# Optimization experiments

Measured on AMD Instinct MI355X. Metric: run time of the kernel, lower is better.

The kernel has to match this reference:

```python
import jax, jax.numpy as jnp
import numpy as np

PAD_TOKEN = -2.0
EPS = 1e-6
NEG_INF = -1.0e9


def _layer_norm(x, gamma, beta):
    mu = jnp.mean(x, axis=-1, keepdims=True)
    var = jnp.mean(jnp.square(x - mu), axis=-1, keepdims=True)
    return (x - mu) * jax.lax.rsqrt(var + EPS) * gamma + beta


def setup_inputs() -> dict:
    key = jax.random.key(0)
    ks = jax.random.split(key, 10)
    B, N, M, D, H, E, O = 128, 32, 384, 256, 8, 32, 256
    S = N + M
    x_pmhc = jax.random.normal(ks[0], (B, S, D), jnp.float32)
    # masks hold raw token values; PAD_TOKEN marks padding positions
    p_len = jax.random.randint(ks[1], (B,), 8, N + 1)
    m_len = jax.random.randint(ks[2], (B,), M // 2, M + 1)
    p_mask = jnp.where(jnp.arange(N)[None, :] < p_len[:, None], 1.0, PAD_TOKEN).astype(jnp.float32)
    m_mask = jnp.where(jnp.arange(M)[None, :] < m_len[:, None], 1.0, PAD_TOKEN).astype(jnp.float32)
    # learned params (keras random_normal init stddev=0.05; random_uniform in [-0.05, 0.05])
    q_proj = 0.05 * jax.random.normal(ks[3], (H, D, E), jnp.float32)
    k_proj = 0.05 * jax.random.normal(ks[4], (H, D, E), jnp.float32)
    v_proj = 0.05 * jax.random.normal(ks[5], (H, D, E), jnp.float32)
    g_proj = jax.random.uniform(ks[6], (H, D, E), jnp.float32, -0.05, 0.05)
    out_w = 0.05 * jax.random.normal(ks[7], (H * E, O), jnp.float32)
    out_b = jnp.zeros((O,), jnp.float32)
    ln1_g = jnp.ones((D,), jnp.float32)
    ln1_b = jnp.zeros((D,), jnp.float32)
    ln2_g = jnp.ones((O,), jnp.float32)
    ln2_b = jnp.zeros((O,), jnp.float32)
    return dict(x_pmhc=x_pmhc, p_mask=p_mask, m_mask=m_mask,
                q_proj=q_proj, k_proj=k_proj, v_proj=v_proj, g_proj=g_proj,
                out_w=out_w, out_b=out_b,
                ln1_g=ln1_g, ln1_b=ln1_b, ln2_g=ln2_g, ln2_b=ln2_b)


def _mask_2d(p, m):
    # p: [B,N] in {0,1}, m: [B,M] in {0,1}
    B, N = p.shape
    M = m.shape[1]
    cross_pm = p[:, :, None] * m[:, None, :]          # [B,N,M]
    cross_mp = m[:, :, None] * p[:, None, :]          # [B,M,N]
    top = jnp.concatenate([jnp.zeros((B, N, N), p.dtype), cross_pm], axis=2)
    bot = jnp.concatenate([cross_mp, jnp.zeros((B, M, M), p.dtype)], axis=2)
    return jnp.concatenate([top, bot], axis=1)        # [B,S,S]


def reference(x_pmhc, p_mask, m_mask, q_proj, k_proj, v_proj, g_proj,
              out_w, out_b, ln1_g, ln1_b, ln2_g, ln2_b):
    H, _, E = q_proj.shape
    B, S, _ = x_pmhc.shape
    scale = 1.0 / jnp.sqrt(jnp.asarray(E, jnp.float32))
    x = _layer_norm(x_pmhc, ln1_g, ln1_b)
    p = jnp.where(p_mask == PAD_TOKEN, 0.0, 1.0)
    m = jnp.where(m_mask == PAD_TOKEN, 0.0, 1.0)
    q = jnp.einsum('bxd,hde->bhxe', x, q_proj)
    k = jnp.einsum('bxd,hde->bhxe', x, k_proj)
    v = jnp.einsum('bxd,hde->bhxe', x, v_proj)
    g = jnp.einsum('bxd,hde->bhxe', x, g_proj)
    att = jnp.einsum('bhxe,bhye->bhxy', q, k) * scale          # [B,H,S,S]
    mask2d = _mask_2d(p, m)                                     # [B,S,S]
    att = jax.nn.softmax(att + ((1.0 - mask2d) * NEG_INF)[:, None], axis=-1)
    att = att * mask2d[:, None]
    out = jnp.einsum('bhxy,bhye->bhxe', att, v)
    out = out * jax.nn.sigmoid(g)
    out = out.transpose(0, 2, 1, 3).reshape(B, S, H * E)
    out = out @ out_w + out_b
    return _layer_norm(out, ln2_g, ln2_b)
```

## Files before the change

kernel.cpp:

```cpp
#include <hip/hip_runtime.h>

typedef unsigned short u16;
typedef __bf16 bf16x8 __attribute__((ext_vector_type(8)));
typedef float f32x4 __attribute__((ext_vector_type(4)));

#define B_    128
#define S_    416
#define NPEP  32
#define MMHC  384
#define D_    256
#define H_    8
#define E_    32
#define O_    256
#define BS_   (B_ * S_)

#define PAD_TOK (-2.0f)
#define SCALE_E 0.17677669529663687f

typedef const __attribute__((address_space(1))) void cg_void;
typedef __attribute__((address_space(3))) void lds_void;

__device__ __forceinline__ float bf2f(u16 u) {
  union { unsigned int i; float f; } x; x.i = ((unsigned int)u) << 16; return x.f;
}
__device__ __forceinline__ u16 f2bf(float f) {
  union { float f; unsigned int i; } x; x.f = f;
  unsigned int i = x.i;
  return (u16)((i + 0x7FFFu + ((i >> 16) & 1u)) >> 16);
}
__device__ __forceinline__ unsigned pk2bf(float lo, float hi) {
  return (unsigned)f2bf(lo) | ((unsigned)f2bf(hi) << 16);
}

__global__ __launch_bounds__(256)
void pack_w(const float* __restrict__ q, const float* __restrict__ k,
            const float* __restrict__ v, const float* __restrict__ g,
            const float* __restrict__ ow, u16* __restrict__ WT, u16* __restrict__ WoT) {
  const int bx = blockIdx.x, t = threadIdx.x;
  if (bx < 1024) {
    const int col = bx;
    const int p = col >> 8, h = (col >> 5) & 7, e = col & 31;
    const float* src = (p == 0) ? q : (p == 1) ? k : (p == 2) ? v : g;
    WT[col * 256 + t] = f2bf(src[(h * 256 + t) * 32 + e]);
  } else {
    const int n = bx - 1024;
    WoT[n * 256 + t] = f2bf(ow[t * 256 + n]);
  }
}

__global__ __launch_bounds__(256)
void ln_f2b(const float* __restrict__ inp, u16* __restrict__ out,
            const float* __restrict__ gam, const float* __restrict__ bet) {
  const int w = threadIdx.x >> 6, lane = threadIdx.x & 63;
  const size_t row = (size_t)blockIdx.x * 4 + w;
  const float4 u = *((const float4*)inp + row * 64 + lane);
  const float x0 = u.x, x1 = u.y, x2 = u.z, x3 = u.w;
  float sum = (x0 + x1) + (x2 + x3);
  float ss  = (x0 * x0 + x1 * x1) + (x2 * x2 + x3 * x3);
  #pragma unroll
  for (int off = 32; off; off >>= 1) {
    sum += __shfl_xor(sum, off);
    ss  += __shfl_xor(ss, off);
  }
  const float mean = sum * 0.00390625f;
  float var = ss * 0.00390625f - mean * mean;
  var = fmaxf(var, 0.0f);
  const float rs = rsqrtf(var + 1e-6f);
  const float4 g4 = *((const float4*)gam + lane);
  const float4 b4 = *((const float4*)bet + lane);
  ushort4 r;
  r.x = f2bf((x0 - mean) * rs * g4.x + b4.x);
  r.y = f2bf((x1 - mean) * rs * g4.y + b4.y);
  r.z = f2bf((x2 - mean) * rs * g4.z + b4.z);
  r.w = f2bf((x3 - mean) * rs * g4.w + b4.w);
  *((ushort4*)out + row * 64 + lane) = r;
}

__global__ __launch_bounds__(256, 2)
void gemm_qkvg(const u16* __restrict__ A, const u16* __restrict__ BT,
               u16* __restrict__ Qh, u16* __restrict__ Kh,
               u16* __restrict__ Vh, u16* __restrict__ Gh) {
  __shared__ __attribute__((aligned(16))) u16 As[128 * 64];
  __shared__ __attribute__((aligned(16))) u16 Bs[128 * 64];
  const int L = blockIdx.x;
  const int m0 = ((L & 7) + 8 * (L >> 6)) * 128;
  const int n0 = ((L >> 3) & 7) * 128;
  const int tid = threadIdx.x;
  const int lane = tid & 63;
  const int w = tid >> 6;
  const int wr = (w >> 1) * 64;
  const int wc = (w & 1) * 64;
  const int mi = lane & 15;
  const int quad = lane >> 4;
  const int rseg = lane >> 3;
  const int gcol = (lane & 7) ^ rseg;
  f32x4 acc[4][4] = {};
  for (int kc = 0; kc < 256; kc += 64) {
    __syncthreads();
    #pragma unroll
    for (int j = 0; j < 4; ++j) {
      const int seg = w * 4 + j;
      const int r = seg * 8 + rseg;
      const u16* ga = &A[(size_t)(m0 + r) * 256 + kc + gcol * 8];
      __builtin_amdgcn_global_load_lds((cg_void*)ga, (lds_void*)&As[seg * 512], 16, 0, 0);
      const u16* gb = &BT[(size_t)(n0 + r) * 256 + kc + gcol * 8];
      __builtin_amdgcn_global_load_lds((cg_void*)gb, (lds_void*)&Bs[seg * 512], 16, 0, 0);
    }
    __syncthreads();
    #pragma unroll
    for (int kt = 0; kt < 2; ++kt) {
      bf16x8 a[4], bb[4];
      #pragma unroll
      for (int i = 0; i < 4; ++i) {
        const int m = wr + i * 16 + mi;
        const int pg = (kt * 4 + quad) ^ (mi & 7);
        a[i] = *(const bf16x8*)&As[m * 64 + pg * 8];
      }
      #pragma unroll
      for (int i = 0; i < 4; ++i) {
        const int n = wc + i * 16 + mi;
        const int pg = (kt * 4 + quad) ^ (mi & 7);
        bb[i] = *(const bf16x8*)&Bs[n * 64 + pg * 8];
      }
      #pragma unroll
      for (int i = 0; i < 4; ++i)
        #pragma unroll
        for (int jn = 0; jn < 4; ++jn)
          acc[i][jn] = __builtin_amdgcn_mfma_f32_16x16x32_bf16(a[i], bb[jn], acc[i][jn], 0, 0, 0);
    }
  }
  u16* dstj[4];
  #pragma unroll
  for (int jn = 0; jn < 4; ++jn) {
    const int colb = n0 + wc + jn * 16;
    const int p = colb >> 8;
    const int h = (colb >> 5) & 7;
    const int e = (colb & 16) + mi;
    u16* bp = (p == 0) ? Qh : (p == 1) ? Kh : (p == 2) ? Vh : Gh;
    dstj[jn] = bp + (size_t)h * BS_ * 32 + e;
  }
  #pragma unroll
  for (int i = 0; i < 4; ++i) {
    const int row = m0 + wr + i * 16 + quad * 4;
    #pragma unroll
    for (int r = 0; r < 4; ++r) {
      #pragma unroll
      for (int jn = 0; jn < 4; ++jn)
        dstj[jn][(size_t)(row + r) * 32] = f2bf(acc[i][jn][r]);
    }
  }
}

__global__ __launch_bounds__(256, 4)
void att_fused(const u16* __restrict__ Qh, const u16* __restrict__ Kh,
               const u16* __restrict__ Vh, const u16* __restrict__ Gh,
               const float* __restrict__ p_mask, const float* __restrict__ m_mask,
               u16* __restrict__ atto) {
  __shared__ __attribute__((aligned(16))) u16 VT[32][392];
  __shared__ __attribute__((aligned(16))) u16 VpT[32][40];
  __shared__ __attribute__((aligned(16))) float pf[32];
  __shared__ __attribute__((aligned(16))) float mfl[384];
  const int bh = blockIdx.x;
  const int b = bh >> 3, h = bh & 7;
  const int t = threadIdx.x;
  const int lane = t & 63, w = t >> 6;
  const int mi = lane & 15, quad = lane >> 4;
  const size_t hb = (size_t)h * BS_ + (size_t)b * S_;

  if (t < 32) pf[t] = (p_mask[b * NPEP + t] == PAD_TOK) ? 0.0f : 1.0f;
  mfl[t] = (m_mask[b * MMHC + t] == PAD_TOK) ? 0.0f : 1.0f;
  if (t < 128) mfl[256 + t] = (m_mask[b * MMHC + 256 + t] == PAD_TOK) ? 0.0f : 1.0f;
  {
    const int y = t >> 3, e0 = (t & 7) * 4;
    const ushort4 u = *(const ushort4*)&Vh[(hb + y) * 32 + e0];
    VpT[e0 + 0][y] = u.x; VpT[e0 + 1][y] = u.y;
    VpT[e0 + 2][y] = u.z; VpT[e0 + 3][y] = u.w;
  }
  #pragma unroll
  for (int i = 0; i < 12; ++i) {
    const int idx = i * 256 + t;
    const int y = idx >> 3, e0 = (idx & 7) * 4;
    const ushort4 u = *(const ushort4*)&Vh[(hb + 32 + y) * 32 + e0];
    VT[e0 + 0][y] = u.x; VT[e0 + 1][y] = u.y;
    VT[e0 + 2][y] = u.z; VT[e0 + 3][y] = u.w;
  }
  __syncthreads();

  const f32x4 fz = {0.0f, 0.0f, 0.0f, 0.0f};
  const int idxA = ((quad & 1) * 2) * 16 + mi;
  const int idxB = idxA + 16;
  const bool hi = quad >= 2;
  union U8 { unsigned u[4]; bf16x8 v; };

  if (w < 2) {
    const bf16x8 aq = *(const bf16x8*)&Qh[(hb + w * 16 + mi) * 32 + quad * 8];
    float lsum = 0.0f;
    f32x4 o0 = fz, o1 = fz;
    #pragma unroll
    for (int ks = 0; ks < 12; ++ks) {
      unsigned pA0, pA1, pB0, pB1;
      {
        const int kt = 2 * ks;
        const bf16x8 bk = *(const bf16x8*)&Kh[(hb + 32 + kt * 16 + mi) * 32 + quad * 8];
        const f32x4 s = __builtin_amdgcn_mfma_f32_16x16x32_bf16(bk, aq, fz, 0, 0, 0);
        const float4 m4 = *(const float4*)&mfl[kt * 16 + quad * 4];
        const float e0 = m4.x * __expf(s[0] * SCALE_E);
        const float e1 = m4.y * __expf(s[1] * SCALE_E);
        const float e2 = m4.z * __expf(s[2] * SCALE_E);
        const float e3 = m4.w * __expf(s[3] * SCALE_E);
        lsum += (e0 + e1) + (e2 + e3);
        pA0 = pk2bf(e0, e1); pA1 = pk2bf(e2, e3);
      }
      {
        const int kt = 2 * ks + 1;
        const bf16x8 bk = *(const bf16x8*)&Kh[(hb + 32 + kt * 16 + mi) * 32 + quad * 8];
        const f32x4 s = __builtin_amdgcn_mfma_f32_16x16x32_bf16(bk, aq, fz, 0, 0, 0);
        const float4 m4 = *(const float4*)&mfl[kt * 16 + quad * 4];
        const float e0 = m4.x * __expf(s[0] * SCALE_E);
        const float e1 = m4.y * __expf(s[1] * SCALE_E);
        const float e2 = m4.z * __expf(s[2] * SCALE_E);
        const float e3 = m4.w * __expf(s[3] * SCALE_E);
        lsum += (e0 + e1) + (e2 + e3);
        pB0 = pk2bf(e0, e1); pB1 = pk2bf(e2, e3);
      }
      const unsigned a00 = __shfl(pA0, idxA), a01 = __shfl(pA1, idxA);
      const unsigned b00 = __shfl(pB0, idxA), b01 = __shfl(pB1, idxA);
      const unsigned a10 = __shfl(pA0, idxB), a11 = __shfl(pA1, idxB);
      const unsigned b10 = __shfl(pB0, idxB), b11 = __shfl(pB1, idxB);
      U8 pf_;
      pf_.u[0] = hi ? b00 : a00;
      pf_.u[1] = hi ? b01 : a01;
      pf_.u[2] = hi ? b10 : a10;
      pf_.u[3] = hi ? b11 : a11;
      const bf16x8 v0 = *(const bf16x8*)&VT[mi][ks * 32 + quad * 8];
      const bf16x8 v1 = *(const bf16x8*)&VT[16 + mi][ks * 32 + quad * 8];
      o0 = __builtin_amdgcn_mfma_f32_16x16x32_bf16(v0, pf_.v, o0, 0, 0, 0);
      o1 = __builtin_amdgcn_mfma_f32_16x16x32_bf16(v1, pf_.v, o1, 0, 0, 0);
    }
    lsum += __shfl_xor(lsum, 16);
    lsum += __shfl_xor(lsum, 32);
    const int prow = w * 16 + mi;
    const float sc = (1.0f / lsum) * pf[prow];
    const ushort4 g0 = *(const ushort4*)&Gh[(hb + prow) * 32 + quad * 4];
    const ushort4 g1 = *(const ushort4*)&Gh[(hb + prow) * 32 + 16 + quad * 4];
    ushort4 r0, r1;
    r0.x = f2bf(o0[0] * sc / (1.0f + __expf(-bf2f(g0.x))));
    r0.y = f2bf(o0[1] * sc / (1.0f + __expf(-bf2f(g0.y))));
    r0.z = f2bf(o0[2] * sc / (1.0f + __expf(-bf2f(g0.z))));
    r0.w = f2bf(o0[3] * sc / (1.0f + __expf(-bf2f(g0.w))));
    r1.x = f2bf(o1[0] * sc / (1.0f + __expf(-bf2f(g1.x))));
    r1.y = f2bf(o1[1] * sc / (1.0f + __expf(-bf2f(g1.y))));
    r1.z = f2bf(o1[2] * sc / (1.0f + __expf(-bf2f(g1.z))));
    r1.w = f2bf(o1[3] * sc / (1.0f + __expf(-bf2f(g1.w))));
    *(ushort4*)&atto[(hb + prow) * 32 + quad * 4] = r0;
    *(ushort4*)&atto[(hb + prow) * 32 + 16 + quad * 4] = r1;
  } else {
    const int wid = w - 2;
    const bf16x8 bk0 = *(const bf16x8*)&Kh[(hb + mi) * 32 + quad * 8];
    const bf16x8 bk1 = *(const bf16x8*)&Kh[(hb + 16 + mi) * 32 + quad * 8];
    const bf16x8 bv0 = *(const bf16x8*)&VpT[mi][quad * 8];
    const bf16x8 bv1 = *(const bf16x8*)&VpT[16 + mi][quad * 8];
    const float4 pfa = *(const float4*)&pf[quad * 4];
    const float4 pfb = *(const float4*)&pf[16 + quad * 4];
    for (int i = 0; i < 12; ++i) {
      const int rloc = (i * 2 + wid) * 16;
      const size_t grow = hb + 32 + rloc + mi;
      const bf16x8 aq = *(const bf16x8*)&Qh[grow * 32 + quad * 8];
      const f32x4 s0 = __builtin_amdgcn_mfma_f32_16x16x32_bf16(bk0, aq, fz, 0, 0, 0);
      const f32x4 s1 = __builtin_amdgcn_mfma_f32_16x16x32_bf16(bk1, aq, fz, 0, 0, 0);
      const float e00 = pfa.x * __expf(s0[0] * SCALE_E);
      const float e01 = pfa.y * __expf(s0[1] * SCALE_E);
      const float e02 = pfa.z * __expf(s0[2] * SCALE_E);
      const float e03 = pfa.w * __expf(s0[3] * SCALE_E);
      const float e10 = pfb.x * __expf(s1[0] * SCALE_E);
      const float e11 = pfb.y * __expf(s1[1] * SCALE_E);
      const float e12 = pfb.z * __expf(s1[2] * SCALE_E);
      const float e13 = pfb.w * __expf(s1[3] * SCALE_E);
      float lsum = ((e00 + e01) + (e02 + e03)) + ((e10 + e11) + (e12 + e13));
      lsum += __shfl_xor(lsum, 16);
      lsum += __shfl_xor(lsum, 32);
      const unsigned pA0 = pk2bf(e00, e01), pA1 = pk2bf(e02, e03);
      const unsigned pB0 = pk2bf(e10, e11), pB1 = pk2bf(e12, e13);
      const unsigned a00 = __shfl(pA0, idxA), a01 = __shfl(pA1, idxA);
      const unsigned b00 = __shfl(pB0, idxA), b01 = __shfl(pB1, idxA);
      const unsigned a10 = __shfl(pA0, idxB), a11 = __shfl(pA1, idxB);
      const unsigned b10 = __shfl(pB0, idxB), b11 = __shfl(pB1, idxB);
      U8 pf_;
      pf_.u[0] = hi ? b00 : a00;
      pf_.u[1] = hi ? b01 : a01;
      pf_.u[2] = hi ? b10 : a10;
      pf_.u[3] = hi ? b11 : a11;
      const f32x4 o0 = __builtin_amdgcn_mfma_f32_16x16x32_bf16(bv0, pf_.v, fz, 0, 0, 0);
      const f32x4 o1 = __builtin_amdgcn_mfma_f32_16x16x32_bf16(bv1, pf_.v, fz, 0, 0, 0);
      const float sc = (1.0f / lsum) * mfl[rloc + mi];
      const ushort4 g0 = *(const ushort4*)&Gh[grow * 32 + quad * 4];
      const ushort4 g1 = *(const ushort4*)&Gh[grow * 32 + 16 + quad * 4];
      ushort4 r0, r1;
      r0.x = f2bf(o0[0] * sc / (1.0f + __expf(-bf2f(g0.x))));
      r0.y = f2bf(o0[1] * sc / (1.0f + __expf(-bf2f(g0.y))));
      r0.z = f2bf(o0[2] * sc / (1.0f + __expf(-bf2f(g0.z))));
      r0.w = f2bf(o0[3] * sc / (1.0f + __expf(-bf2f(g0.w))));
      r1.x = f2bf(o1[0] * sc / (1.0f + __expf(-bf2f(g1.x))));
      r1.y = f2bf(o1[1] * sc / (1.0f + __expf(-bf2f(g1.y))));
      r1.z = f2bf(o1[2] * sc / (1.0f + __expf(-bf2f(g1.z))));
      r1.w = f2bf(o1[3] * sc / (1.0f + __expf(-bf2f(g1.w))));
      *(ushort4*)&atto[grow * 32 + quad * 4] = r0;
      *(ushort4*)&atto[grow * 32 + 16 + quad * 4] = r1;
    }
  }
}

__global__ __launch_bounds__(512, 2)
void gemm2_ln(const u16* __restrict__ A, const u16* __restrict__ BT,
              float* __restrict__ out, const float* __restrict__ bias,
              const float* __restrict__ gam, const float* __restrict__ bet) {
  __shared__ __attribute__((aligned(16))) u16 As[128 * 64];
  __shared__ __attribute__((aligned(16))) u16 Bs[256 * 64];
  __shared__ float rsum[128][4];
  __shared__ float rssq[128][4];
  __shared__ float mean_s[128], rstd_s[128];
  const int m0 = blockIdx.x * 128;
  const int tid = threadIdx.x;
  const int lane = tid & 63;
  const int w = tid >> 6;
  const int wr = (w >> 2) * 64;
  const int wc = (w & 3) * 64;
  const int mi = lane & 15;
  const int quad = lane >> 4;
  const int rseg = lane >> 3;
  const int gcol = (lane & 7) ^ rseg;
  f32x4 acc[4][4] = {};
  for (int kc = 0; kc < 256; kc += 64) {
    __syncthreads();
    #pragma unroll
    for (int j = 0; j < 2; ++j) {
      const int seg = w * 2 + j;
      const int r = seg * 8 + rseg;
      const int c = kc + gcol * 8;
      const u16* ga = &A[((size_t)(c >> 5) * BS_ + (m0 + r)) * 32 + (c & 31)];
      __builtin_amdgcn_global_load_lds((cg_void*)ga, (lds_void*)&As[seg * 512], 16, 0, 0);
    }
    #pragma unroll
    for (int j = 0; j < 4; ++j) {
      const int seg = w * 4 + j;
      const int r = seg * 8 + rseg;
      const u16* gb = &BT[(size_t)r * 256 + kc + gcol * 8];
      __builtin_amdgcn_global_load_lds((cg_void*)gb, (lds_void*)&Bs[seg * 512], 16, 0, 0);
    }
    __syncthreads();
    #pragma unroll
    for (int kt = 0; kt < 2; ++kt) {
      bf16x8 a[4], bb[4];
      #pragma unroll
      for (int i = 0; i < 4; ++i) {
        const int m = wr + i * 16 + mi;
        const int pg = (kt * 4 + quad) ^ (mi & 7);
        a[i] = *(const bf16x8*)&As[m * 64 + pg * 8];
      }
      #pragma unroll
      for (int i = 0; i < 4; ++i) {
        const int n = wc + i * 16 + mi;
        const int pg = (kt * 4 + quad) ^ (mi & 7);
        bb[i] = *(const bf16x8*)&Bs[n * 64 + pg * 8];
      }
      #pragma unroll
      for (int i = 0; i < 4; ++i)
        #pragma unroll
        for (int jn = 0; jn < 4; ++jn)
          acc[i][jn] = __builtin_amdgcn_mfma_f32_16x16x32_bf16(a[i], bb[jn], acc[i][jn], 0, 0, 0);
    }
  }
  float bia[4];
  #pragma unroll
  for (int jn = 0; jn < 4; ++jn) bia[jn] = bias[wc + jn * 16 + mi];
  #pragma unroll
  for (int i = 0; i < 4; ++i) {
    #pragma unroll
    for (int r = 0; r < 4; ++r) {
      float s = 0.0f, qq = 0.0f;
      #pragma unroll
      for (int jn = 0; jn < 4; ++jn) {
        const float v = acc[i][jn][r] + bia[jn];
        s += v; qq += v * v;
      }
      #pragma unroll
      for (int off = 1; off < 16; off <<= 1) {
        s  += __shfl_xor(s, off);
        qq += __shfl_xor(qq, off);
      }
      if (mi == 0) {
        const int rl = wr + i * 16 + quad * 4 + r;
        rsum[rl][w & 3] = s;
        rssq[rl][w & 3] = qq;
      }
    }
  }
  __syncthreads();
  if (tid < 128) {
    const float s = rsum[tid][0] + rsum[tid][1] + rsum[tid][2] + rsum[tid][3];
    const float qq = rssq[tid][0] + rssq[tid][1] + rssq[tid][2] + rssq[tid][3];
    const float mean = s * 0.00390625f;
    float var = qq * 0.00390625f - mean * mean;
    var = fmaxf(var, 0.0f);
    mean_s[tid] = mean;
    rstd_s[tid] = rsqrtf(var + 1e-6f);
  }
  __syncthreads();
  #pragma unroll
  for (int jn = 0; jn < 4; ++jn) {
    const int col = wc + jn * 16 + mi;
    const float gv = gam[col], bv = bet[col];
    #pragma unroll
    for (int i = 0; i < 4; ++i) {
      #pragma unroll
      for (int r = 0; r < 4; ++r) {
        const int rl = wr + i * 16 + quad * 4 + r;
        const float v = acc[i][jn][r] + bia[jn];
        out[(size_t)(m0 + rl) * 256 + col] = (v - mean_s[rl]) * rstd_s[rl] * gv + bv;
      }
    }
  }
}

extern "C" void kernel_launch(void* const* d_in, const int* in_sizes, int n_in,
                              void* d_out, int out_size, void* d_ws, size_t ws_size,
                              hipStream_t stream) {
  const float* x      = (const float*)d_in[0];
  const float* p_mask = (const float*)d_in[1];
  const float* m_mask = (const float*)d_in[2];
  const float* q_proj = (const float*)d_in[3];
  const float* k_proj = (const float*)d_in[4];
  const float* v_proj = (const float*)d_in[5];
  const float* g_proj = (const float*)d_in[6];
  const float* out_w  = (const float*)d_in[7];
  const float* out_b  = (const float*)d_in[8];
  const float* ln1_g  = (const float*)d_in[9];
  const float* ln1_b  = (const float*)d_in[10];
  const float* ln2_g  = (const float*)d_in[11];
  const float* ln2_b  = (const float*)d_in[12];

  char* ws = (char*)d_ws;
  u16* WT   = (u16*)(ws);
  u16* WoT  = (u16*)(ws + 524288);
  u16* attx = (u16*)(ws + 655360);
  u16* Qh   = (u16*)(ws + 27918336);
  u16* Kh   = (u16*)(ws + 55181312);
  u16* Vh   = (u16*)(ws + 82444288);
  u16* Gh   = (u16*)(ws + 109707264);
  float* outp = (float*)d_out;

  hipLaunchKernelGGL(pack_w, dim3(1280), dim3(256), 0, stream,
                     q_proj, k_proj, v_proj, g_proj, out_w, WT, WoT);
  hipLaunchKernelGGL(ln_f2b, dim3(BS_ / 4), dim3(256), 0, stream,
                     x, attx, ln1_g, ln1_b);
  hipLaunchKernelGGL(gemm_qkvg, dim3(8 * (BS_ / 128)), dim3(256), 0, stream,
                     attx, WT, Qh, Kh, Vh, Gh);
  hipLaunchKernelGGL(att_fused, dim3(B_ * H_), dim3(256), 0, stream,
                     Qh, Kh, Vh, Gh, p_mask, m_mask, attx);
  hipLaunchKernelGGL(gemm2_ln, dim3(BS_ / 128), dim3(512), 0, stream,
                     attx, WoT, outp, out_b, ln2_g, ln2_b);
}
```

Before: 223.8 us.

## Double-buffer QKVG GEMM LDS tiles and merge weight packing with LayerNorm

Merges the weight-packing kernel and the first LayerNorm kernel into one launch, with block ranges picking the job. This removes one launch and its gap. The QKVG GEMM now double-buffers its A and B LDS tiles, so the next k-chunk's global-to-LDS load is issued before the MFMAs on the current chunk, and one barrier per iteration is dropped. LDS use doubles to 64KB per block, which may cut occupancy against the launch-bounds hint of two blocks per CU.

```diff
diff --git a/kernel.cpp b/kernel.cpp
--- a/kernel.cpp
+++ b/kernel.cpp
@@ -33,27 +33,27 @@
 }
 
 __global__ __launch_bounds__(256)
-void pack_w(const float* __restrict__ q, const float* __restrict__ k,
-            const float* __restrict__ v, const float* __restrict__ g,
-            const float* __restrict__ ow, u16* __restrict__ WT, u16* __restrict__ WoT) {
+void prep(const float* __restrict__ q, const float* __restrict__ k,
+          const float* __restrict__ v, const float* __restrict__ g,
+          const float* __restrict__ ow, u16* __restrict__ WT, u16* __restrict__ WoT,
+          const float* __restrict__ x, u16* __restrict__ xln,
+          const float* __restrict__ gam, const float* __restrict__ bet) {
   const int bx = blockIdx.x, t = threadIdx.x;
   if (bx < 1024) {
     const int col = bx;
     const int p = col >> 8, h = (col >> 5) & 7, e = col & 31;
     const float* src = (p == 0) ? q : (p == 1) ? k : (p == 2) ? v : g;
     WT[col * 256 + t] = f2bf(src[(h * 256 + t) * 32 + e]);
-  } else {
+    return;
+  }
+  if (bx < 1280) {
     const int n = bx - 1024;
     WoT[n * 256 + t] = f2bf(ow[t * 256 + n]);
-  }
-}
-
-__global__ __launch_bounds__(256)
-void ln_f2b(const float* __restrict__ inp, u16* __restrict__ out,
-            const float* __restrict__ gam, const float* __restrict__ bet) {
-  const int w = threadIdx.x >> 6, lane = threadIdx.x & 63;
-  const size_t row = (size_t)blockIdx.x * 4 + w;
-  const float4 u = *((const float4*)inp + row * 64 + lane);
+    return;
+  }
+  const int w = t >> 6, lane = t & 63;
+  const size_t row = (size_t)(bx - 1280) * 4 + w;
+  const float4 u = *((const float4*)x + row * 64 + lane);
   const float x0 = u.x, x1 = u.y, x2 = u.z, x3 = u.w;
   float sum = (x0 + x1) + (x2 + x3);
   float ss  = (x0 * x0 + x1 * x1) + (x2 * x2 + x3 * x3);
@@ -73,15 +73,15 @@
   r.y = f2bf((x1 - mean) * rs * g4.y + b4.y);
   r.z = f2bf((x2 - mean) * rs * g4.z + b4.z);
   r.w = f2bf((x3 - mean) * rs * g4.w + b4.w);
-  *((ushort4*)out + row * 64 + lane) = r;
+  *((ushort4*)xln + row * 64 + lane) = r;
 }
 
 __global__ __launch_bounds__(256, 2)
 void gemm_qkvg(const u16* __restrict__ A, const u16* __restrict__ BT,
                u16* __restrict__ Qh, u16* __restrict__ Kh,
                u16* __restrict__ Vh, u16* __restrict__ Gh) {
-  __shared__ __attribute__((aligned(16))) u16 As[128 * 64];
-  __shared__ __attribute__((aligned(16))) u16 Bs[128 * 64];
+  __shared__ __attribute__((aligned(16))) u16 As[2][128 * 64];
+  __shared__ __attribute__((aligned(16))) u16 Bs[2][128 * 64];
   const int L = blockIdx.x;
   const int m0 = ((L & 7) + 8 * (L >> 6)) * 128;
   const int n0 = ((L >> 3) & 7) * 128;
@@ -94,19 +94,29 @@
   const int quad = lane >> 4;
   const int rseg = lane >> 3;
   const int gcol = (lane & 7) ^ rseg;
+
+#define STAGE_G1(buf, kc)                                                      \
+  {                                                                            \
+    _Pragma("unroll")                                                          \
+    for (int j = 0; j < 4; ++j) {                                              \
+      const int seg = w * 4 + j;                                               \
+      const int r = seg * 8 + rseg;                                            \
+      const u16* ga = &A[(size_t)(m0 + r) * 256 + (kc) + gcol * 8];            \
+      __builtin_amdgcn_global_load_lds((cg_void*)ga,                           \
+          (lds_void*)&As[buf][seg * 512], 16, 0, 0);                           \
+      const u16* gb = &BT[(size_t)(n0 + r) * 256 + (kc) + gcol * 8];           \
+      __builtin_amdgcn_global_load_lds((cg_void*)gb,                           \
+          (lds_void*)&Bs[buf][seg * 512], 16, 0, 0);                           \
+    }                                                                          \
+  }
+
   f32x4 acc[4][4] = {};
-  for (int kc = 0; kc < 256; kc += 64) {
-    __syncthreads();
-    #pragma unroll
-    for (int j = 0; j < 4; ++j) {
-      const int seg = w * 4 + j;
-      const int r = seg * 8 + rseg;
-      const u16* ga = &A[(size_t)(m0 + r) * 256 + kc + gcol * 8];
-      __builtin_amdgcn_global_load_lds((cg_void*)ga, (lds_void*)&As[seg * 512], 16, 0, 0);
-      const u16* gb = &BT[(size_t)(n0 + r) * 256 + kc + gcol * 8];
-      __builtin_amdgcn_global_load_lds((cg_void*)gb, (lds_void*)&Bs[seg * 512], 16, 0, 0);
-    }
-    __syncthreads();
+  STAGE_G1(0, 0);
+  __syncthreads();
+  #pragma unroll
+  for (int kt8 = 0; kt8 < 4; ++kt8) {
+    const int cur = kt8 & 1;
+    if (kt8 < 3) STAGE_G1(cur ^ 1, (kt8 + 1) * 64);
     #pragma unroll
     for (int kt = 0; kt < 2; ++kt) {
       bf16x8 a[4], bb[4];
@@ -114,13 +124,13 @@
       for (int i = 0; i < 4; ++i) {
         const int m = wr + i * 16 + mi;
         const int pg = (kt * 4 + quad) ^ (mi & 7);
-        a[i] = *(const bf16x8*)&As[m * 64 + pg * 8];
+        a[i] = *(const bf16x8*)&As[cur][m * 64 + pg * 8];
       }
       #pragma unroll
       for (int i = 0; i < 4; ++i) {
         const int n = wc + i * 16 + mi;
         const int pg = (kt * 4 + quad) ^ (mi & 7);
-        bb[i] = *(const bf16x8*)&Bs[n * 64 + pg * 8];
+        bb[i] = *(const bf16x8*)&Bs[cur][n * 64 + pg * 8];
       }
       #pragma unroll
       for (int i = 0; i < 4; ++i)
@@ -128,7 +138,9 @@
         for (int jn = 0; jn < 4; ++jn)
           acc[i][jn] = __builtin_amdgcn_mfma_f32_16x16x32_bf16(a[i], bb[jn], acc[i][jn], 0, 0, 0);
     }
-  }
+    if (kt8 < 3) __syncthreads();
+  }
+#undef STAGE_G1
   u16* dstj[4];
   #pragma unroll
   for (int jn = 0; jn < 4; ++jn) {
@@ -449,9 +461,8 @@
   u16* Gh   = (u16*)(ws + 109707264);
   float* outp = (float*)d_out;
 
-  hipLaunchKernelGGL(pack_w, dim3(1280), dim3(256), 0, stream,
-                     q_proj, k_proj, v_proj, g_proj, out_w, WT, WoT);
-  hipLaunchKernelGGL(ln_f2b, dim3(BS_ / 4), dim3(256), 0, stream,
+  hipLaunchKernelGGL(prep, dim3(1280 + BS_ / 4), dim3(256), 0, stream,
+                     q_proj, k_proj, v_proj, g_proj, out_w, WT, WoT,
                      x, attx, ln1_g, ln1_b);
   hipLaunchKernelGGL(gemm_qkvg, dim3(8 * (BS_ / 128)), dim3(256), 0, stream,
                      attx, WT, Qh, Kh, Vh, Gh);
```

Result: slower. 228.4 us (+2.1%).
